# Kernel optimization log

Measured on AMD Instinct MI355X. Metric: run time of the kernel, lower is better.

The kernel has to match this reference:

```python
import jax, jax.numpy as jnp
import numpy as np

N_NODES = 50000
N_EDGES = 800000
IN_C = 128
OUT_C = 128
ALPHA = 0.2  # leaky_relu negative slope (args.egat_alpha)
EDGE_K = 3   # edgefeat width, fixed by W_out in-dim = 3*out_channels


def setup_inputs() -> dict:
    key = jax.random.key(0)
    k = jax.random.split(key, 7)
    h = jax.random.normal(k[0], (N_NODES, IN_C), dtype=jnp.float32)
    edge_index = jax.random.randint(k[1], (2, N_EDGES), 0, N_NODES, dtype=jnp.int64)
    edgefeat = jax.random.uniform(k[2], (N_EDGES, EDGE_K), dtype=jnp.float32)
    # glorot-initialized linear weights (stored as [in, out] for x @ W)
    def glorot(kk, fan_in, fan_out):
        lim = jnp.sqrt(6.0 / (fan_in + fan_out)).astype(jnp.float32)
        return jax.random.uniform(kk, (fan_in, fan_out), jnp.float32, -lim, lim)
    W = glorot(k[3], IN_C, OUT_C)
    a1 = glorot(k[4], OUT_C, 1)
    a2 = glorot(k[5], OUT_C, 1)
    W_out = glorot(k[6], EDGE_K * OUT_C, OUT_C)
    return {"h": h, "edge_index": edge_index, "edgefeat": edgefeat,
            "W": W, "a1": a1, "a2": a2, "W_out": W_out}


def reference(h, edge_index, edgefeat, W, a1, a2, W_out):
    src = edge_index[0]  # j: message source
    dst = edge_index[1]  # i: aggregation target
    n = h.shape[0]

    Wh = h @ W                                   # [N, C]
    s1 = Wh @ a1                                 # [N, 1] alpha_j scores
    s2 = Wh @ a2                                 # [N, 1] alpha_i scores

    # edge_update: leaky_relu(alpha_j + alpha_i) * edge_attr, then edge softmax over dst
    e = s1[src] + s2[dst]                        # [E, 1]
    e = jnp.where(e >= 0, e, ALPHA * e)
    alpha = e * edgefeat                         # [E, 3]
    m = jax.ops.segment_max(alpha, dst, num_segments=n)      # [N, 3]
    m = jnp.where(jnp.isfinite(m), m, 0.0)
    ex = jnp.exp(alpha - m[dst])
    denom = jax.ops.segment_sum(ex, dst, num_segments=n)     # [N, 3]
    att = ex / (denom[dst] + 1e-16)              # [E, 3] (dropout p applied at eval -> identity)

    # message: outer product att[E,3] x x_j[E,C] -> [E, 3C] -> W_out -> [E, C]
    x_j = Wh[src]                                # [E, C]
    msg = (att[:, :, None] * x_j[:, None, :]).reshape(att.shape[0], EDGE_K * Wh.shape[1])
    msg = msg @ W_out                            # [E, C]

    # aggregate: sum at destination nodes
    out = jax.ops.segment_sum(msg, dst, num_segments=n)      # [N, C]
    return out
```

## Files before the change

### kernel.cpp

```cpp
#include <hip/hip_runtime.h>
#include <hip/hip_bf16.h>

#define ALPHA 0.2f
typedef unsigned int uint32;
typedef __attribute__((ext_vector_type(8))) short short8;
typedef __attribute__((ext_vector_type(4))) float f32x4;

static __device__ __forceinline__ unsigned short f2bf(float f) {
    unsigned int u = __float_as_uint(f);
    u += 0x7fffu + ((u >> 16) & 1u);
    return (unsigned short)(u >> 16);
}
static __device__ __forceinline__ uint32 pk2bf(float lo, float hi) {
    return (uint32)f2bf(lo) | ((uint32)f2bf(hi) << 16);
}
static __device__ __forceinline__ float bflo(uint32 u) { return __uint_as_float(u << 16); }
static __device__ __forceinline__ float bfhi(uint32 u) { return __uint_as_float(u & 0xffff0000u); }

__global__ __launch_bounds__(256) void prep2_kernel(const float* __restrict__ W,
                                                    const float* __restrict__ Wout,
                                                    const float* __restrict__ a1,
                                                    const float* __restrict__ a2,
                                                    unsigned short* __restrict__ WT2,
                                                    float* __restrict__ w1f,
                                                    float* __restrict__ w2f) {
    __shared__ float WT_lds[129 * 128];
    __shared__ float Wos[128 * 16];
    const int tid = threadIdx.x;
    for (int i = tid; i < 16384; i += 256) {
        int j = i >> 7, c = i & 127;
        WT_lds[c * 129 + j] = W[i];
    }
    if (blockIdx.x < 24) {
        int s = blockIdx.x >> 3, nb = blockIdx.x & 7;
        for (int i = tid; i < 2048; i += 256) {
            int c = i >> 4, q = i & 15;
            Wos[i] = Wout[(size_t)(s * 128 + c) * 128 + nb * 16 + q];
        }
        __syncthreads();
        int j = tid & 127, nh = tid >> 7;
        float acc[8];
#pragma unroll
        for (int p = 0; p < 8; ++p) acc[p] = 0.f;
        for (int c = 0; c < 128; ++c) {
            float w = WT_lds[c * 129 + j];
#pragma unroll
            for (int p = 0; p < 8; ++p) acc[p] += w * Wos[c * 16 + nh * 8 + p];
        }
#pragma unroll
        for (int p = 0; p < 8; ++p) {
            int n = nb * 16 + nh * 8 + p;
            WT2[((size_t)s * 128 + n) * 128 + j] = f2bf(acc[p]);
        }
    } else {
        __syncthreads();
        if (tid < 128) {
            float acc1 = 0.f, acc2 = 0.f;
            for (int c = 0; c < 128; ++c) {
                float w = WT_lds[c * 129 + tid];
                acc1 += w * a1[c];
                acc2 += w * a2[c];
            }
            w1f[tid] = acc1;
            w2f[tid] = acc2;
        }
    }
}

__global__ __launch_bounds__(256) void mmy2_kernel(const float* __restrict__ h,
                                                   const unsigned short* __restrict__ WT2,
                                                   const float* __restrict__ w1f,
                                                   const float* __restrict__ w2f,
                                                   unsigned short* __restrict__ Yb,
                                                   float* __restrict__ s1,
                                                   float* __restrict__ s2, int M) {
    __shared__ unsigned short As[128 * 128];
    __shared__ unsigned short Bs[128 * 128];
    __shared__ float ws1[128], ws2[128];
    const int tid  = threadIdx.x;
    const int lane = tid & 63;
    const int w    = tid >> 6;
    const int row0 = blockIdx.x * 128;

    if (tid < 128) ws1[tid] = w1f[tid];
    else           ws2[tid - 128] = w2f[tid - 128];
    __syncthreads();

    const float4* h4 = (const float4*)h;
    float sp1[8], sp2[8];
#pragma unroll
    for (int m = 0; m < 8; ++m) { sp1[m] = 0.f; sp2[m] = 0.f; }
#pragma unroll
    for (int m = 0; m < 8; ++m) {
        int i = m * 256 + tid;
        int r = i >> 4, g = i & 15;
        int rg = row0 + r;
        float4 va = make_float4(0.f, 0.f, 0.f, 0.f), vb = va;
        if (rg < M) {
            va = h4[(size_t)rg * 32 + g * 2];
            vb = h4[(size_t)rg * 32 + g * 2 + 1];
        }
        float4 wa1 = *(const float4*)(ws1 + g * 8);
        float4 wb1 = *(const float4*)(ws1 + g * 8 + 4);
        float4 wa2 = *(const float4*)(ws2 + g * 8);
        float4 wb2 = *(const float4*)(ws2 + g * 8 + 4);
        sp1[m] += va.x * wa1.x + va.y * wa1.y + va.z * wa1.z + va.w * wa1.w
                + vb.x * wb1.x + vb.y * wb1.y + vb.z * wb1.z + vb.w * wb1.w;
        sp2[m] += va.x * wa2.x + va.y * wa2.y + va.z * wa2.z + va.w * wa2.w
                + vb.x * wb2.x + vb.y * wb2.y + vb.z * wb2.z + vb.w * wb2.w;
        uint4 u;
        u.x = pk2bf(va.x, va.y); u.y = pk2bf(va.z, va.w);
        u.z = pk2bf(vb.x, vb.y); u.w = pk2bf(vb.z, vb.w);
        *(uint4*)(As + r * 128 + ((g ^ (r & 15)) * 8)) = u;
    }
#pragma unroll
    for (int m = 0; m < 8; ++m) {
#pragma unroll
        for (int off = 1; off < 16; off <<= 1) {
            sp1[m] += __shfl_xor(sp1[m], off);
            sp2[m] += __shfl_xor(sp2[m], off);
        }
    }
    if ((tid & 15) == 0) {
#pragma unroll
        for (int m = 0; m < 8; ++m) {
            int rg = row0 + m * 16 + (tid >> 4);
            if (rg < M) { s1[rg] = sp1[m]; s2[rg] = sp2[m]; }
        }
    }

    const int ml   = lane & 15;
    const int quad = lane >> 4;
    for (int ks = 0; ks < 3; ++ks) {
        __syncthreads();
#pragma unroll
        for (int m = 0; m < 8; ++m) {
            int i = m * 256 + tid;
            int n = i >> 4, g = i & 15;
            uint4 v = *(const uint4*)(WT2 + (size_t)ks * 16384 + n * 128 + g * 8);
            *(uint4*)(Bs + n * 128 + ((g ^ (n & 15)) * 8)) = v;
        }
        __syncthreads();

        f32x4 acc[2][8];
#pragma unroll
        for (int mt = 0; mt < 2; ++mt)
#pragma unroll
            for (int nt = 0; nt < 8; ++nt) acc[mt][nt] = (f32x4){0.f, 0.f, 0.f, 0.f};
#pragma unroll
        for (int kc = 0; kc < 4; ++kc) {
            int gl = ((kc * 4 + quad) ^ ml) * 8;
            short8 af0 = *(const short8*)(As + (w * 32 + ml) * 128 + gl);
            short8 af1 = *(const short8*)(As + (w * 32 + 16 + ml) * 128 + gl);
#pragma unroll
            for (int nt = 0; nt < 8; ++nt) {
                short8 bf = *(const short8*)(Bs + (nt * 16 + ml) * 128 + gl);
                acc[0][nt] = __builtin_amdgcn_mfma_f32_16x16x32_bf16(af0, bf, acc[0][nt], 0, 0, 0);
                acc[1][nt] = __builtin_amdgcn_mfma_f32_16x16x32_bf16(af1, bf, acc[1][nt], 0, 0, 0);
            }
        }
#pragma unroll
        for (int mt = 0; mt < 2; ++mt) {
            int rbase = row0 + w * 32 + mt * 16 + quad * 4;
#pragma unroll
            for (int r = 0; r < 4; ++r) {
                int rg = rbase + r;
                if (rg >= M) continue;
                unsigned short* yrow = Yb + (size_t)rg * 384 + ks * 128 + ml;
#pragma unroll
                for (int nt = 0; nt < 8; ++nt)
                    yrow[nt * 16] = f2bf(acc[mt][nt][r]);
            }
        }
    }
}

__global__ __launch_bounds__(256) void hist_kernel(const int* __restrict__ ei,
                                                   int* __restrict__ counts,
                                                   int* __restrict__ eslot, int E) {
    int e = blockIdx.x * blockDim.x + threadIdx.x;
    if (e < E) eslot[e] = atomicAdd(&counts[ei[E + e]], 1);
}

__global__ __launch_bounds__(256) void scan1_kernel(const int* __restrict__ counts,
                                                    int* __restrict__ csum, int N) {
    __shared__ int wsums[4];
    const int tid = threadIdx.x, lane = tid & 63, wv = tid >> 6;
    int i0 = blockIdx.x * 1024 + tid * 4;
    int s = 0;
    if (i0 + 3 < N) {
        int4 v = *(const int4*)(counts + i0);
        s = v.x + v.y + v.z + v.w;
    } else {
        for (int q = 0; q < 4; ++q) if (i0 + q < N) s += counts[i0 + q];
    }
#pragma unroll
    for (int off = 32; off > 0; off >>= 1) s += __shfl_down(s, off);
    if (lane == 0) wsums[wv] = s;
    __syncthreads();
    if (tid == 0) csum[blockIdx.x] = wsums[0] + wsums[1] + wsums[2] + wsums[3];
}

__global__ __launch_bounds__(256) void scan3b_kernel(const int* __restrict__ counts,
                                                     const int* __restrict__ csum,
                                                     int* __restrict__ rowptr,
                                                     int N, int E, int nchunk) {
    __shared__ int wsums[4];
    __shared__ int coff_s;
    const int tid = threadIdx.x, lane = tid & 63, wv = tid >> 6;
    if (tid < 64) {
        int v = (tid < nchunk) ? csum[tid] : 0;
        int incl = v;
#pragma unroll
        for (int off = 1; off < 64; off <<= 1) {
            int t = __shfl_up(incl, off);
            if (tid >= off) incl += t;
        }
        if (tid == blockIdx.x) coff_s = incl - v;
        if (blockIdx.x == 0 && tid == 0) rowptr[N] = E;
    }
    int i0 = blockIdx.x * 1024 + tid * 4;
    int v0 = 0, v1 = 0, v2 = 0, v3 = 0;
    if (i0 + 3 < N) {
        int4 v = *(const int4*)(counts + i0);
        v0 = v.x; v1 = v.y; v2 = v.z; v3 = v.w;
    } else {
        if (i0 + 0 < N) v0 = counts[i0 + 0];
        if (i0 + 1 < N) v1 = counts[i0 + 1];
        if (i0 + 2 < N) v2 = counts[i0 + 2];
        if (i0 + 3 < N) v3 = counts[i0 + 3];
    }
    int tt = v0 + v1 + v2 + v3;
    int incl = tt;
#pragma unroll
    for (int off = 1; off < 64; off <<= 1) {
        int t = __shfl_up(incl, off);
        if (lane >= off) incl += t;
    }
    if (lane == 63) wsums[wv] = incl;
    __syncthreads();
    int woff = 0;
    for (int w2 = 0; w2 < wv; ++w2) woff += wsums[w2];
    int base = coff_s + woff + (incl - tt);
    if (i0 + 0 < N) rowptr[i0 + 0] = base;
    if (i0 + 1 < N) rowptr[i0 + 1] = base + v0;
    if (i0 + 2 < N) rowptr[i0 + 2] = base + v0 + v1;
    if (i0 + 3 < N) rowptr[i0 + 3] = base + v0 + v1 + v2;
}

__global__ __launch_bounds__(256) void scatter_kernel(const int* __restrict__ ei,
                                                      const float* __restrict__ ef,
                                                      const float* __restrict__ s1,
                                                      const float* __restrict__ s2,
                                                      const int* __restrict__ rowptr,
                                                      const int* __restrict__ eslot,
                                                      float4* __restrict__ rec, int E) {
    int e = blockIdx.x * blockDim.x + threadIdx.x;
    if (e >= E) return;
    int src = ei[e];
    int dst = ei[E + e];
    float s = s1[src] + s2[dst];
    s = (s >= 0.f) ? s : ALPHA * s;
    float ex0 = __expf(s * ef[e * 3 + 0]);
    float ex1 = __expf(s * ef[e * 3 + 1]);
    float ex2 = __expf(s * ef[e * 3 + 2]);
    int pos = rowptr[dst] + eslot[e];
    rec[pos] = make_float4(ex0, ex1, ex2, __int_as_float(src));
}

__global__ __launch_bounds__(256) void agg_kernel(const float4* __restrict__ rec,
                                                  const int* __restrict__ rowptr,
                                                  const uint32* __restrict__ Yu,
                                                  float* __restrict__ out, int N) {
    int node = (blockIdx.x * blockDim.x + threadIdx.x) >> 6;
    int lane = threadIdx.x & 63;
    if (node >= N) return;
    int beg = rowptr[node], end = rowptr[node + 1];

    float d0 = 0.f, d1 = 0.f, d2 = 0.f;
    for (int jb = beg + lane; jb < end; jb += 64) {
        float4 r = rec[jb];
        d0 += r.x; d1 += r.y; d2 += r.z;
    }
#pragma unroll
    for (int off = 32; off > 0; off >>= 1) {
        d0 += __shfl_xor(d0, off);
        d1 += __shfl_xor(d1, off);
        d2 += __shfl_xor(d2, off);
    }
    float inv0 = 1.f / (d0 + 1e-16f);
    float inv1 = 1.f / (d1 + 1e-16f);
    float inv2 = 1.f / (d2 + 1e-16f);

    float a0 = 0.f, a1 = 0.f;
    int j = beg;
    for (; j + 7 < end; j += 8) {
        float4 r[8]; const uint32* p[8]; uint32 u[8][3];
#pragma unroll
        for (int t = 0; t < 8; ++t) {
            r[t] = rec[j + t];
            p[t] = Yu + (size_t)__float_as_int(r[t].w) * 192;
        }
#pragma unroll
        for (int t = 0; t < 8; ++t) {
            u[t][0] = p[t][lane]; u[t][1] = p[t][64 + lane]; u[t][2] = p[t][128 + lane];
        }
#pragma unroll
        for (int t = 0; t < 8; ++t) {
            float w0 = r[t].x * inv0, w1 = r[t].y * inv1, w2 = r[t].z * inv2;
            a0 += w0 * bflo(u[t][0]) + w1 * bflo(u[t][1]) + w2 * bflo(u[t][2]);
            a1 += w0 * bfhi(u[t][0]) + w1 * bfhi(u[t][1]) + w2 * bfhi(u[t][2]);
        }
    }
    for (; j + 1 < end; j += 2) {
        float4 r0 = rec[j], r1 = rec[j + 1];
        const uint32* p0 = Yu + (size_t)__float_as_int(r0.w) * 192;
        const uint32* p1 = Yu + (size_t)__float_as_int(r1.w) * 192;
        uint32 u00 = p0[lane], u01 = p0[64 + lane], u02 = p0[128 + lane];
        uint32 u10 = p1[lane], u11 = p1[64 + lane], u12 = p1[128 + lane];
        float w00 = r0.x * inv0, w01 = r0.y * inv1, w02 = r0.z * inv2;
        float w10 = r1.x * inv0, w11 = r1.y * inv1, w12 = r1.z * inv2;
        a0 += w00 * bflo(u00) + w01 * bflo(u01) + w02 * bflo(u02);
        a1 += w00 * bfhi(u00) + w01 * bfhi(u01) + w02 * bfhi(u02);
        a0 += w10 * bflo(u10) + w11 * bflo(u11) + w12 * bflo(u12);
        a1 += w10 * bfhi(u10) + w11 * bfhi(u11) + w12 * bfhi(u12);
    }
    if (j < end) {
        float4 r0 = rec[j];
        const uint32* p0 = Yu + (size_t)__float_as_int(r0.w) * 192;
        uint32 u00 = p0[lane], u01 = p0[64 + lane], u02 = p0[128 + lane];
        float w00 = r0.x * inv0, w01 = r0.y * inv1, w02 = r0.z * inv2;
        a0 += w00 * bflo(u00) + w01 * bflo(u01) + w02 * bflo(u02);
        a1 += w00 * bfhi(u00) + w01 * bfhi(u01) + w02 * bfhi(u02);
    }
    ((float2*)(out + (size_t)node * 128))[lane] = make_float2(a0, a1);
}

extern "C" void kernel_launch(void* const* d_in, const int* in_sizes, int n_in,
                              void* d_out, int out_size, void* d_ws, size_t ws_size,
                              hipStream_t stream) {
    const float* h    = (const float*)d_in[0];
    const int*   ei   = (const int*)d_in[1];
    const float* ef   = (const float*)d_in[2];
    const float* W    = (const float*)d_in[3];
    const float* a1   = (const float*)d_in[4];
    const float* a2   = (const float*)d_in[5];
    const float* Wout = (const float*)d_in[6];
    float*       out  = (float*)d_out;

    const int N = in_sizes[0] / 128;
    const int E = in_sizes[2] / 3;
    const int nchunk = (N + 1023) / 1024;

    float4* rec = (float4*)d_ws;
    unsigned short* Yb  = (unsigned short*)(rec + E);
    unsigned short* WT2 = Yb + (size_t)N * 384;
    float* w1f  = (float*)(WT2 + 3 * 128 * 128);
    float* w2f  = w1f + 128;
    float* s1   = w2f + 128;
    float* s2   = s1 + N;
    int* counts = (int*)(s2 + N);
    int* rowptr = counts + N;
    int* eslot  = rowptr + N + 1;
    int* csum   = eslot + E;

    hipMemsetAsync(counts, 0, (size_t)N * sizeof(int), stream);

    hist_kernel<<<(E + 255) / 256, 256, 0, stream>>>(ei, counts, eslot, E);
    prep2_kernel<<<25, 256, 0, stream>>>(W, Wout, a1, a2, WT2, w1f, w2f);
    mmy2_kernel<<<(N + 127) / 128, 256, 0, stream>>>(h, WT2, w1f, w2f, Yb, s1, s2, N);
    scan1_kernel<<<nchunk, 256, 0, stream>>>(counts, csum, N);
    scan3b_kernel<<<nchunk, 256, 0, stream>>>(counts, csum, rowptr, N, E, nchunk);
    scatter_kernel<<<(E + 255) / 256, 256, 0, stream>>>(ei, ef, s1, s2, rowptr, eslot, rec, E);
    agg_kernel<<<(N * 64 + 255) / 256, 256, 0, stream>>>(rec, rowptr, (const uint32*)Yb, out, N);
}
```

Measured before the change: 262.0 us.

## Use nontemporal loads/stores, fuse scan kernels, shrink agg unroll to four

Global loads and stores in the matmul, histogram, scatter and aggregation kernels now use nontemporal builtins so streamed data bypasses cache retention. The two-pass scan is merged into one kernel: each block recomputes the sum of all preceding counts itself, which removes a launch at the cost of redundant reads. The aggregation loop is unrolled by four instead of eight, which lowers register pressure but leaves fewer gathers in flight. Nontemporal hints on rec and Yb, which are re-read by later kernels, could hurt L2 reuse.

```diff
diff --git a/kernel.cpp b/kernel.cpp
--- a/kernel.cpp
+++ b/kernel.cpp
@@ -5,6 +5,7 @@
 typedef unsigned int uint32;
 typedef __attribute__((ext_vector_type(8))) short short8;
 typedef __attribute__((ext_vector_type(4))) float f32x4;
+typedef __attribute__((ext_vector_type(2))) float f32x2;
 
 static __device__ __forceinline__ unsigned short f2bf(float f) {
     unsigned int u = __float_as_uint(f);
@@ -86,7 +87,7 @@
     else           ws2[tid - 128] = w2f[tid - 128];
     __syncthreads();
 
-    const float4* h4 = (const float4*)h;
+    const f32x4* h4 = (const f32x4*)h;
     float sp1[8], sp2[8];
 #pragma unroll
     for (int m = 0; m < 8; ++m) { sp1[m] = 0.f; sp2[m] = 0.f; }
@@ -95,10 +96,10 @@
         int i = m * 256 + tid;
         int r = i >> 4, g = i & 15;
         int rg = row0 + r;
-        float4 va = make_float4(0.f, 0.f, 0.f, 0.f), vb = va;
+        f32x4 va = (f32x4){0.f, 0.f, 0.f, 0.f}, vb = va;
         if (rg < M) {
-            va = h4[(size_t)rg * 32 + g * 2];
-            vb = h4[(size_t)rg * 32 + g * 2 + 1];
+            va = __builtin_nontemporal_load(h4 + (size_t)rg * 32 + g * 2);
+            vb = __builtin_nontemporal_load(h4 + (size_t)rg * 32 + g * 2 + 1);
         }
         float4 wa1 = *(const float4*)(ws1 + g * 8);
         float4 wb1 = *(const float4*)(ws1 + g * 8 + 4);
@@ -169,7 +170,7 @@
                 unsigned short* yrow = Yb + (size_t)rg * 384 + ks * 128 + ml;
 #pragma unroll
                 for (int nt = 0; nt < 8; ++nt)
-                    yrow[nt * 16] = f2bf(acc[mt][nt][r]);
+                    __builtin_nontemporal_store(f2bf(acc[mt][nt][r]), yrow + nt * 16);
             }
         }
     }
@@ -179,46 +180,33 @@
                                                    int* __restrict__ counts,
                                                    int* __restrict__ eslot, int E) {
     int e = blockIdx.x * blockDim.x + threadIdx.x;
-    if (e < E) eslot[e] = atomicAdd(&counts[ei[E + e]], 1);
-}
-
-__global__ __launch_bounds__(256) void scan1_kernel(const int* __restrict__ counts,
-                                                    int* __restrict__ csum, int N) {
+    if (e < E) {
+        int d = __builtin_nontemporal_load(ei + E + e);
+        int slot = atomicAdd(&counts[d], 1);
+        __builtin_nontemporal_store(slot, eslot + e);
+    }
+}
+
+__global__ __launch_bounds__(256) void scan_fused_kernel(const int* __restrict__ counts,
+                                                         int* __restrict__ rowptr,
+                                                         int N, int E) {
     __shared__ int wsums[4];
+    __shared__ int base_s;
     const int tid = threadIdx.x, lane = tid & 63, wv = tid >> 6;
-    int i0 = blockIdx.x * 1024 + tid * 4;
-    int s = 0;
-    if (i0 + 3 < N) {
-        int4 v = *(const int4*)(counts + i0);
-        s = v.x + v.y + v.z + v.w;
-    } else {
-        for (int q = 0; q < 4; ++q) if (i0 + q < N) s += counts[i0 + q];
-    }
-#pragma unroll
-    for (int off = 32; off > 0; off >>= 1) s += __shfl_down(s, off);
-    if (lane == 0) wsums[wv] = s;
-    __syncthreads();
-    if (tid == 0) csum[blockIdx.x] = wsums[0] + wsums[1] + wsums[2] + wsums[3];
-}
-
-__global__ __launch_bounds__(256) void scan3b_kernel(const int* __restrict__ counts,
-                                                     const int* __restrict__ csum,
-                                                     int* __restrict__ rowptr,
-                                                     int N, int E, int nchunk) {
-    __shared__ int wsums[4];
-    __shared__ int coff_s;
-    const int tid = threadIdx.x, lane = tid & 63, wv = tid >> 6;
-    if (tid < 64) {
-        int v = (tid < nchunk) ? csum[tid] : 0;
-        int incl = v;
-#pragma unroll
-        for (int off = 1; off < 64; off <<= 1) {
-            int t = __shfl_up(incl, off);
-            if (tid >= off) incl += t;
-        }
-        if (tid == blockIdx.x) coff_s = incl - v;
-        if (blockIdx.x == 0 && tid == 0) rowptr[N] = E;
-    }
+
+    const int limit = blockIdx.x * 1024;
+    int acc = 0;
+    for (int i = tid * 4; i < limit; i += 1024) {
+        int4 v = *(const int4*)(counts + i);
+        acc += v.x + v.y + v.z + v.w;
+    }
+#pragma unroll
+    for (int off = 32; off > 0; off >>= 1) acc += __shfl_down(acc, off);
+    if (lane == 0) wsums[wv] = acc;
+    __syncthreads();
+    if (tid == 0) base_s = wsums[0] + wsums[1] + wsums[2] + wsums[3];
+    __syncthreads();
+
     int i0 = blockIdx.x * 1024 + tid * 4;
     int v0 = 0, v1 = 0, v2 = 0, v3 = 0;
     if (i0 + 3 < N) {
@@ -237,15 +225,17 @@
         int t = __shfl_up(incl, off);
         if (lane >= off) incl += t;
     }
+    __syncthreads();
     if (lane == 63) wsums[wv] = incl;
     __syncthreads();
     int woff = 0;
     for (int w2 = 0; w2 < wv; ++w2) woff += wsums[w2];
-    int base = coff_s + woff + (incl - tt);
+    int base = base_s + woff + (incl - tt);
     if (i0 + 0 < N) rowptr[i0 + 0] = base;
     if (i0 + 1 < N) rowptr[i0 + 1] = base + v0;
     if (i0 + 2 < N) rowptr[i0 + 2] = base + v0 + v1;
     if (i0 + 3 < N) rowptr[i0 + 3] = base + v0 + v1 + v2;
+    if (blockIdx.x == 0 && tid == 0) rowptr[N] = E;
 }
 
 __global__ __launch_bounds__(256) void scatter_kernel(const int* __restrict__ ei,
@@ -254,21 +244,26 @@
                                                       const float* __restrict__ s2,
                                                       const int* __restrict__ rowptr,
                                                       const int* __restrict__ eslot,
-                                                      float4* __restrict__ rec, int E) {
+                                                      f32x4* __restrict__ rec, int E) {
     int e = blockIdx.x * blockDim.x + threadIdx.x;
     if (e >= E) return;
-    int src = ei[e];
-    int dst = ei[E + e];
+    int src = __builtin_nontemporal_load(ei + e);
+    int dst = __builtin_nontemporal_load(ei + E + e);
     float s = s1[src] + s2[dst];
     s = (s >= 0.f) ? s : ALPHA * s;
-    float ex0 = __expf(s * ef[e * 3 + 0]);
-    float ex1 = __expf(s * ef[e * 3 + 1]);
-    float ex2 = __expf(s * ef[e * 3 + 2]);
-    int pos = rowptr[dst] + eslot[e];
-    rec[pos] = make_float4(ex0, ex1, ex2, __int_as_float(src));
-}
-
-__global__ __launch_bounds__(256) void agg_kernel(const float4* __restrict__ rec,
+    float f0 = __builtin_nontemporal_load(ef + e * 3 + 0);
+    float f1 = __builtin_nontemporal_load(ef + e * 3 + 1);
+    float f2 = __builtin_nontemporal_load(ef + e * 3 + 2);
+    f32x4 r;
+    r.x = __expf(s * f0);
+    r.y = __expf(s * f1);
+    r.z = __expf(s * f2);
+    r.w = __int_as_float(src);
+    int pos = rowptr[dst] + __builtin_nontemporal_load(eslot + e);
+    __builtin_nontemporal_store(r, rec + pos);
+}
+
+__global__ __launch_bounds__(256) void agg_kernel(const f32x4* __restrict__ rec,
                                                   const int* __restrict__ rowptr,
                                                   const uint32* __restrict__ Yu,
                                                   float* __restrict__ out, int N) {
@@ -279,7 +274,7 @@
 
     float d0 = 0.f, d1 = 0.f, d2 = 0.f;
     for (int jb = beg + lane; jb < end; jb += 64) {
-        float4 r = rec[jb];
+        f32x4 r = __builtin_nontemporal_load(rec + jb);
         d0 += r.x; d1 += r.y; d2 += r.z;
     }
 #pragma unroll
@@ -294,46 +289,42 @@
 
     float a0 = 0.f, a1 = 0.f;
     int j = beg;
-    for (; j + 7 < end; j += 8) {
-        float4 r[8]; const uint32* p[8]; uint32 u[8][3];
-#pragma unroll
-        for (int t = 0; t < 8; ++t) {
-            r[t] = rec[j + t];
-            p[t] = Yu + (size_t)__float_as_int(r[t].w) * 192;
-        }
-#pragma unroll
-        for (int t = 0; t < 8; ++t) {
-            u[t][0] = p[t][lane]; u[t][1] = p[t][64 + lane]; u[t][2] = p[t][128 + lane];
-        }
-#pragma unroll
-        for (int t = 0; t < 8; ++t) {
-            float w0 = r[t].x * inv0, w1 = r[t].y * inv1, w2 = r[t].z * inv2;
-            a0 += w0 * bflo(u[t][0]) + w1 * bflo(u[t][1]) + w2 * bflo(u[t][2]);
-            a1 += w0 * bfhi(u[t][0]) + w1 * bfhi(u[t][1]) + w2 * bfhi(u[t][2]);
-        }
-    }
-    for (; j + 1 < end; j += 2) {
-        float4 r0 = rec[j], r1 = rec[j + 1];
+    for (; j + 3 < end; j += 4) {
+        f32x4 r0 = __builtin_nontemporal_load(rec + j);
+        f32x4 r1 = __builtin_nontemporal_load(rec + j + 1);
+        f32x4 r2 = __builtin_nontemporal_load(rec + j + 2);
+        f32x4 r3 = __builtin_nontemporal_load(rec + j + 3);
         const uint32* p0 = Yu + (size_t)__float_as_int(r0.w) * 192;
         const uint32* p1 = Yu + (size_t)__float_as_int(r1.w) * 192;
+        const uint32* p2 = Yu + (size_t)__float_as_int(r2.w) * 192;
+        const uint32* p3 = Yu + (size_t)__float_as_int(r3.w) * 192;
         uint32 u00 = p0[lane], u01 = p0[64 + lane], u02 = p0[128 + lane];
         uint32 u10 = p1[lane], u11 = p1[64 + lane], u12 = p1[128 + lane];
+        uint32 u20 = p2[lane], u21 = p2[64 + lane], u22 = p2[128 + lane];
+        uint32 u30 = p3[lane], u31 = p3[64 + lane], u32 = p3[128 + lane];
         float w00 = r0.x * inv0, w01 = r0.y * inv1, w02 = r0.z * inv2;
         float w10 = r1.x * inv0, w11 = r1.y * inv1, w12 = r1.z * inv2;
+        float w20 = r2.x * inv0, w21 = r2.y * inv1, w22 = r2.z * inv2;
+        float w30 = r3.x * inv0, w31 = r3.y * inv1, w32 = r3.z * inv2;
         a0 += w00 * bflo(u00) + w01 * bflo(u01) + w02 * bflo(u02);
         a1 += w00 * bfhi(u00) + w01 * bfhi(u01) + w02 * bfhi(u02);
         a0 += w10 * bflo(u10) + w11 * bflo(u11) + w12 * bflo(u12);
         a1 += w10 * bfhi(u10) + w11 * bfhi(u11) + w12 * bfhi(u12);
-    }
-    if (j < end) {
-        float4 r0 = rec[j];
+        a0 += w20 * bflo(u20) + w21 * bflo(u21) + w22 * bflo(u22);
+        a1 += w20 * bfhi(u20) + w21 * bfhi(u21) + w22 * bfhi(u22);
+        a0 += w30 * bflo(u30) + w31 * bflo(u31) + w32 * bflo(u32);
+        a1 += w30 * bfhi(u30) + w31 * bfhi(u31) + w32 * bfhi(u32);
+    }
+    for (; j < end; ++j) {
+        f32x4 r0 = __builtin_nontemporal_load(rec + j);
         const uint32* p0 = Yu + (size_t)__float_as_int(r0.w) * 192;
         uint32 u00 = p0[lane], u01 = p0[64 + lane], u02 = p0[128 + lane];
         float w00 = r0.x * inv0, w01 = r0.y * inv1, w02 = r0.z * inv2;
         a0 += w00 * bflo(u00) + w01 * bflo(u01) + w02 * bflo(u02);
         a1 += w00 * bfhi(u00) + w01 * bfhi(u01) + w02 * bfhi(u02);
     }
-    ((float2*)(out + (size_t)node * 128))[lane] = make_float2(a0, a1);
+    f32x2 o; o.x = a0; o.y = a1;
+    __builtin_nontemporal_store(o, (f32x2*)(out + (size_t)node * 128) + lane);
 }
 
 extern "C" void kernel_launch(void* const* d_in, const int* in_sizes, int n_in,
@@ -352,7 +343,7 @@
     const int E = in_sizes[2] / 3;
     const int nchunk = (N + 1023) / 1024;
 
-    float4* rec = (float4*)d_ws;
+    f32x4* rec = (f32x4*)d_ws;
     unsigned short* Yb  = (unsigned short*)(rec + E);
     unsigned short* WT2 = Yb + (size_t)N * 384;
     float* w1f  = (float*)(WT2 + 3 * 128 * 128);
@@ -362,15 +353,13 @@
     int* counts = (int*)(s2 + N);
     int* rowptr = counts + N;
     int* eslot  = rowptr + N + 1;
-    int* csum   = eslot + E;
-
-    hipMemsetAsync(counts, 0, (size_t)N * sizeof(int), stream);
+
+    (void)hipMemsetAsync(counts, 0, (size_t)N * sizeof(int), stream);
 
     hist_kernel<<<(E + 255) / 256, 256, 0, stream>>>(ei, counts, eslot, E);
     prep2_kernel<<<25, 256, 0, stream>>>(W, Wout, a1, a2, WT2, w1f, w2f);
     mmy2_kernel<<<(N + 127) / 128, 256, 0, stream>>>(h, WT2, w1f, w2f, Yb, s1, s2, N);
-    scan1_kernel<<<nchunk, 256, 0, stream>>>(counts, csum, N);
-    scan3b_kernel<<<nchunk, 256, 0, stream>>>(counts, csum, rowptr, N, E, nchunk);
+    scan_fused_kernel<<<nchunk, 256, 0, stream>>>(counts, rowptr, N, E);
     scatter_kernel<<<(E + 255) / 256, 256, 0, stream>>>(ei, ef, s1, s2, rowptr, eslot, rec, E);
     agg_kernel<<<(N * 64 + 255) / 256, 256, 0, stream>>>(rec, rowptr, (const uint32*)Yb, out, N);
 }
```

Result: slower. 282.5 us (+7.8%).
